# Performance work log

Measured on AMD Instinct MI355X. Metric: run time of the kernel, lower is better.

Reference implementation:

```python
import jax, jax.numpy as jnp
import numpy as np

HIDDEN = 512
BATCH = 32
SEQ = 4096


def setup_inputs() -> dict:
    key = jax.random.key(0)
    ks = jax.random.split(key, 8)
    s = 1.0 / np.sqrt(HIDDEN)
    return {
        "encoder_outputs": jax.random.normal(ks[0], (BATCH, SEQ, HIDDEN), jnp.float32),
        "decoder_hidden": jax.random.normal(ks[1], (BATCH, HIDDEN), jnp.float32),
        "W_enc": jax.random.uniform(ks[2], (HIDDEN, HIDDEN), jnp.float32, -s, s),
        "b_enc": jax.random.uniform(ks[3], (HIDDEN,), jnp.float32, -s, s),
        "W_dec": jax.random.uniform(ks[4], (HIDDEN, HIDDEN), jnp.float32, -s, s),
        "b_dec": jax.random.uniform(ks[5], (HIDDEN,), jnp.float32, -s, s),
        "W_v": jax.random.uniform(ks[6], (HIDDEN, 1), jnp.float32, -s, s),
        "b_v": jax.random.uniform(ks[7], (1,), jnp.float32, -s, s),
    }


def reference(encoder_outputs, decoder_hidden, W_enc, b_enc, W_dec, b_dec, W_v, b_v):
    # (b, s, h) projected encoder states
    enc_proj = jnp.einsum("bsh,hk->bsk", encoder_outputs, W_enc) + b_enc
    # (b, 1, h) projected decoder state, broadcast-added over seq
    dec_proj = (decoder_hidden @ W_dec + b_dec)[:, None, :]
    # score: (b, s, 1)
    score = jnp.tanh(enc_proj + dec_proj) @ W_v + b_v
    attention_weights = jax.nn.softmax(score, axis=1)  # softmax over seq_len
    # context: (b, h) weighted sum of encoder outputs
    context = jnp.sum(attention_weights * encoder_outputs, axis=1)
    return context, jnp.squeeze(attention_weights, -1)
```

## Files before the change

kernel.cpp:

```cpp
#include <hip/hip_runtime.h>
#include <hip/hip_bf16.h>

typedef __attribute__((ext_vector_type(8))) short bf16x8;
typedef __attribute__((ext_vector_type(4))) float f32x4;

#define HID 512
#define NB 32
#define SEQL 4096
#define BM 64
#define BK 32
#define NKC 16
#define NBLK 2048

#define WS_BP    0
#define WS_DPROJ (512*1024)
#define WS_SUM   (576*1024)

__device__ __forceinline__ short f2bf(float f) {
    unsigned u = __float_as_uint(f);
    unsigned r = (u + 0x7fffu + ((u >> 16) & 1u)) >> 16;
    return (short)r;
}

__device__ __forceinline__ float fast_tanh(float x) {
    float e = __expf(2.0f * x);
    float r = __builtin_amdgcn_rcpf(e + 1.0f);
    return 1.0f - 2.0f * r;
}

__device__ __forceinline__ void async16(const void* g, void* l) {
    __builtin_amdgcn_global_load_lds((__attribute__((address_space(1))) void*)(g),
                                     (__attribute__((address_space(3))) void*)(l),
                                     16, 0, 0);
}

__global__ void k_pre(const float* __restrict__ We, short* __restrict__ Bp,
                      const float* __restrict__ dec, const float* __restrict__ Wd,
                      const float* __restrict__ be, const float* __restrict__ bd,
                      float* __restrict__ dproj, float* __restrict__ out,
                      float* __restrict__ sumacc) {
    const int blk = blockIdx.x, t = threadIdx.x;
    if (blk < 128) {
        int tid  = blk * 256 + t;
        int lane = tid & 63;
        int nt   = (tid >> 6) & 31;
        int kc   = tid >> 11;
        int k0   = kc * 32 + (lane >> 4) * 8;
        int n    = nt * 16 + (lane & 15);
        bf16x8 v;
#pragma unroll
        for (int j = 0; j < 8; ++j) v[j] = f2bf(We[(size_t)(k0 + j) * HID + n]);
        *(bf16x8*)&Bp[(size_t)tid * 8] = v;
    } else if (blk < 192) {
        int bid = blk - 128;
        if (bid == 0 && t < NB) sumacc[t] = 0.f;
        int kl = t & 31, bq = t >> 5;
        int k  = (bid & 15) * 32 + kl;
        int b  = (bid >> 4) * 8 + bq;
        float a = be[k] + bd[k];
        const float* dr = dec + (size_t)b * HID;
#pragma unroll 8
        for (int h = 0; h < HID; ++h)
            a += dr[h] * Wd[(size_t)h * HID + k];
        dproj[(size_t)b * HID + k] = a;
    } else {
        out[(blk - 192) * 256 + t] = 0.f;
    }
}

__global__ __launch_bounds__(256, 2)
void k_main(const float* __restrict__ E, const short* __restrict__ Bp,
            const float* __restrict__ dproj, const float* __restrict__ Wv,
            float* __restrict__ out, float* __restrict__ sumacc) {
    __shared__ short As[2][BM][BK + 8];
    __shared__ short Bs[2][BK * HID];
    __shared__ float fbuf[640];
    __shared__ float pbuf[BM];

    const int tid  = threadIdx.x;
    const int wave = tid >> 6, lane = tid & 63;
    const int quad = lane >> 4, l15 = lane & 15;
    const int bid  = blockIdx.x;
    const int row0 = bid * BM;
    const int b    = bid >> 6;

    f32x4 acc[4][8];
#pragma unroll
    for (int r = 0; r < 4; ++r)
#pragma unroll
        for (int c = 0; c < 8; ++c) acc[r][c] = (f32x4){0.f, 0.f, 0.f, 0.f};

    const int arow = tid >> 2, akq = tid & 3;
    const float* aptr = E + (size_t)(row0 + arow) * HID + akq * 8;

    {
        const short* bsrc = Bp;
#pragma unroll
        for (int i = 0; i < 8; ++i) {
            int off = (i * 4 + wave) * 512;
            async16(bsrc + off + lane * 8, &Bs[0][off]);
        }
        float4 a0 = *(const float4*)(aptr);
        float4 a1 = *(const float4*)(aptr + 4);
        bf16x8 av;
        av[0] = f2bf(a0.x); av[1] = f2bf(a0.y); av[2] = f2bf(a0.z); av[3] = f2bf(a0.w);
        av[4] = f2bf(a1.x); av[5] = f2bf(a1.y); av[6] = f2bf(a1.z); av[7] = f2bf(a1.w);
        *(bf16x8*)&As[0][arow][akq * 8] = av;
    }

    int cur = 0;
    for (int kc = 0; kc < NKC; ++kc) {
        const int nxt = cur ^ 1;
        __syncthreads();

        float4 a0, a1;
        const bool pf = (kc + 1 < NKC);
        if (pf) {
            a0 = *(const float4*)(aptr + (kc + 1) * 32);
            a1 = *(const float4*)(aptr + (kc + 1) * 32 + 4);
            const short* bsrc = Bp + (size_t)(kc + 1) * 16384;
#pragma unroll
            for (int i = 0; i < 8; ++i) {
                int off = (i * 4 + wave) * 512;
                async16(bsrc + off + lane * 8, &Bs[nxt][off]);
            }
        }

        bf16x8 fa[4];
#pragma unroll
        for (int r = 0; r < 4; ++r) fa[r] = *(bf16x8*)&As[cur][r * 16 + l15][quad * 8];
#pragma unroll
        for (int c = 0; c < 8; ++c) {
            int nt = wave * 8 + c;
            bf16x8 fb = *(bf16x8*)&Bs[cur][(nt * 64 + lane) * 8];
#pragma unroll
            for (int r = 0; r < 4; ++r)
                acc[r][c] = __builtin_amdgcn_mfma_f32_16x16x32_bf16(fa[r], fb, acc[r][c], 0, 0, 0);
        }

        if (pf) {
            bf16x8 av;
            av[0] = f2bf(a0.x); av[1] = f2bf(a0.y); av[2] = f2bf(a0.z); av[3] = f2bf(a0.w);
            av[4] = f2bf(a1.x); av[5] = f2bf(a1.y); av[6] = f2bf(a1.z); av[7] = f2bf(a1.w);
            *(bf16x8*)&As[nxt][arow][akq * 8] = av;
        }
        cur = nxt;
    }

    float part[4][4];
#pragma unroll
    for (int r = 0; r < 4; ++r)
#pragma unroll
        for (int g = 0; g < 4; ++g) part[r][g] = 0.f;
    const float* dp = dproj + (size_t)b * HID;
#pragma unroll
    for (int c = 0; c < 8; ++c) {
        int col = wave * 128 + c * 16 + l15;
        float dv = dp[col];
        float wv = Wv[col];
#pragma unroll
        for (int r = 0; r < 4; ++r)
#pragma unroll
            for (int g = 0; g < 4; ++g)
                part[r][g] += fast_tanh(acc[r][c][g] + dv) * wv;
    }
#pragma unroll
    for (int r = 0; r < 4; ++r)
#pragma unroll
        for (int g = 0; g < 4; ++g) {
            float v = part[r][g];
            v += __shfl_xor(v, 1); v += __shfl_xor(v, 2);
            v += __shfl_xor(v, 4); v += __shfl_xor(v, 8);
            part[r][g] = v;
        }
    if (l15 == 0) {
#pragma unroll
        for (int r = 0; r < 4; ++r)
#pragma unroll
            for (int g = 0; g < 4; ++g)
                fbuf[wave * 64 + r * 16 + quad * 4 + g] = part[r][g];
    }
    __syncthreads();
    if (tid < 64) {
        float s  = fbuf[tid] + fbuf[64 + tid] + fbuf[128 + tid] + fbuf[192 + tid];
        float pv = __expf(s);
        pbuf[tid] = pv;
        out[(size_t)NB * HID + row0 + tid] = pv;
        float t2 = pv;
        t2 += __shfl_xor(t2, 1);  t2 += __shfl_xor(t2, 2);  t2 += __shfl_xor(t2, 4);
        t2 += __shfl_xor(t2, 8);  t2 += __shfl_xor(t2, 16); t2 += __shfl_xor(t2, 32);
        if (tid == 0) atomicAdd(&sumacc[b], t2);
    }
    __syncthreads();

    const int hq = tid & 127, rh = tid >> 7;
    const float4* E4 = (const float4*)E;
    size_t cbase = (size_t)(row0 + rh * 32) * (HID / 4) + hq;
    float4 ca = {0.f, 0.f, 0.f, 0.f};
#pragma unroll 4
    for (int rr = 0; rr < 32; ++rr) {
        float w  = pbuf[rh * 32 + rr];
        float4 e = E4[cbase + (size_t)rr * (HID / 4)];
        ca.x += w * e.x; ca.y += w * e.y; ca.z += w * e.z; ca.w += w * e.w;
    }
    if (rh == 1) {
        fbuf[hq] = ca.x; fbuf[128 + hq] = ca.y; fbuf[256 + hq] = ca.z; fbuf[384 + hq] = ca.w;
    }
    __syncthreads();
    if (rh == 0) {
        ca.x += fbuf[hq]; ca.y += fbuf[128 + hq]; ca.z += fbuf[256 + hq]; ca.w += fbuf[384 + hq];
        float* cg = out + (size_t)b * HID + hq * 4;
        atomicAdd(cg + 0, ca.x); atomicAdd(cg + 1, ca.y);
        atomicAdd(cg + 2, ca.z); atomicAdd(cg + 3, ca.w);
    }
}

__global__ void k_finish(float* __restrict__ out, const float* __restrict__ sumacc) {
    int b = blockIdx.x, t = threadIdx.x;
    float rs = 1.0f / sumacc[b];
    for (int i = t; i < HID; i += 256)
        out[(size_t)b * HID + i] *= rs;
    float* ow = out + (size_t)NB * HID + (size_t)b * SEQL;
    for (int i = t; i < SEQL; i += 256)
        ow[i] *= rs;
}

extern "C" void kernel_launch(void* const* d_in, const int* in_sizes, int n_in,
                              void* d_out, int out_size, void* d_ws, size_t ws_size,
                              hipStream_t stream) {
    const float* E   = (const float*)d_in[0];
    const float* dec = (const float*)d_in[1];
    const float* We  = (const float*)d_in[2];
    const float* be  = (const float*)d_in[3];
    const float* Wd  = (const float*)d_in[4];
    const float* bd  = (const float*)d_in[5];
    const float* Wv  = (const float*)d_in[6];
    float* out = (float*)d_out;
    char*  ws  = (char*)d_ws;
    short* Bp     = (short*)(ws + WS_BP);
    float* dproj  = (float*)(ws + WS_DPROJ);
    float* sumacc = (float*)(ws + WS_SUM);

    k_pre<<<256, 256, 0, stream>>>(We, Bp, dec, Wd, be, bd, dproj, out, sumacc);
    k_main<<<NBLK, 256, 0, stream>>>(E, Bp, dproj, Wv, out, sumacc);
    k_finish<<<NB, 256, 0, stream>>>(out, sumacc);
}
```

Baseline: 492.0 us.

## Deepen encoder-tile prefetch to two stages and split decoder projection across more blocks

The main GEMM loop now keeps two register stages of encoder loads in flight, issuing the load for chunk kc+2 while chunk kc is computed, and fully unrolls the k-loop so the buffer indices are compile-time constants. The decoder projection in the prep kernel is split over 512 blocks, with each block reducing its hidden dimension across 8 thread groups through shared memory, replacing 64 blocks that each ran a serial 512-long dot product. The aim is to hide global-load latency in the main kernel and shorten the prep kernel's critical path. The cost is more live registers, which could hurt occupancy at 2 blocks per CU, plus one redundant wrap-around load of chunk 0 in the last iterations.

```diff
diff --git a/kernel.cpp b/kernel.cpp
--- a/kernel.cpp
+++ b/kernel.cpp
@@ -51,20 +51,31 @@
 #pragma unroll
         for (int j = 0; j < 8; ++j) v[j] = f2bf(We[(size_t)(k0 + j) * HID + n]);
         *(bf16x8*)&Bp[(size_t)tid * 8] = v;
-    } else if (blk < 192) {
-        int bid = blk - 128;
-        if (bid == 0 && t < NB) sumacc[t] = 0.f;
-        int kl = t & 31, bq = t >> 5;
-        int k  = (bid & 15) * 32 + kl;
-        int b  = (bid >> 4) * 8 + bq;
-        float a = be[k] + bd[k];
+    } else if (blk < 640) {
+        __shared__ float red[8][33];
+        int bid2 = blk - 128;
+        int b  = bid2 >> 4, kg = bid2 & 15;
+        int kl = t & 31,    hc = t >> 5;
+        int k  = kg * 32 + kl;
         const float* dr = dec + (size_t)b * HID;
+        float a = 0.f;
 #pragma unroll 8
-        for (int h = 0; h < HID; ++h)
+        for (int j = 0; j < 64; ++j) {
+            int h = hc * 64 + j;
             a += dr[h] * Wd[(size_t)h * HID + k];
-        dproj[(size_t)b * HID + k] = a;
+        }
+        red[hc][kl] = a;
+        __syncthreads();
+        if (hc == 0) {
+            float s = be[k] + bd[k];
+#pragma unroll
+            for (int c = 0; c < 8; ++c) s += red[c][kl];
+            dproj[(size_t)b * HID + k] = s;
+        }
     } else {
-        out[(blk - 192) * 256 + t] = 0.f;
+        int bz = blk - 640;
+        out[bz * 256 + t] = 0.f;
+        if (bz == 0 && t < NB) sumacc[t] = 0.f;
     }
 }
 
@@ -93,6 +104,12 @@
     const int arow = tid >> 2, akq = tid & 3;
     const float* aptr = E + (size_t)(row0 + arow) * HID + akq * 8;
 
+    float4 pa0[2], pa1[2];
+
+    pa0[0] = *(const float4*)(aptr);
+    pa1[0] = *(const float4*)(aptr + 4);
+    pa0[1] = *(const float4*)(aptr + 32);
+    pa1[1] = *(const float4*)(aptr + 36);
     {
         const short* bsrc = Bp;
 #pragma unroll
@@ -100,24 +117,23 @@
             int off = (i * 4 + wave) * 512;
             async16(bsrc + off + lane * 8, &Bs[0][off]);
         }
-        float4 a0 = *(const float4*)(aptr);
-        float4 a1 = *(const float4*)(aptr + 4);
         bf16x8 av;
-        av[0] = f2bf(a0.x); av[1] = f2bf(a0.y); av[2] = f2bf(a0.z); av[3] = f2bf(a0.w);
-        av[4] = f2bf(a1.x); av[5] = f2bf(a1.y); av[6] = f2bf(a1.z); av[7] = f2bf(a1.w);
+        av[0] = f2bf(pa0[0].x); av[1] = f2bf(pa0[0].y); av[2] = f2bf(pa0[0].z); av[3] = f2bf(pa0[0].w);
+        av[4] = f2bf(pa1[0].x); av[5] = f2bf(pa1[0].y); av[6] = f2bf(pa1[0].z); av[7] = f2bf(pa1[0].w);
         *(bf16x8*)&As[0][arow][akq * 8] = av;
     }
 
-    int cur = 0;
+#pragma unroll
     for (int kc = 0; kc < NKC; ++kc) {
-        const int nxt = cur ^ 1;
+        const int cur = kc & 1, nxt = cur ^ 1;
         __syncthreads();
 
-        float4 a0, a1;
-        const bool pf = (kc + 1 < NKC);
-        if (pf) {
-            a0 = *(const float4*)(aptr + (kc + 1) * 32);
-            a1 = *(const float4*)(aptr + (kc + 1) * 32 + 4);
+        {
+            const int src = (kc + 2 < NKC) ? (kc + 2) : 0;
+            pa0[kc & 1] = *(const float4*)(aptr + src * 32);
+            pa1[kc & 1] = *(const float4*)(aptr + src * 32 + 4);
+        }
+        if (kc + 1 < NKC) {
             const short* bsrc = Bp + (size_t)(kc + 1) * 16384;
 #pragma unroll
             for (int i = 0; i < 8; ++i) {
@@ -138,13 +154,13 @@
                 acc[r][c] = __builtin_amdgcn_mfma_f32_16x16x32_bf16(fa[r], fb, acc[r][c], 0, 0, 0);
         }
 
-        if (pf) {
+        if (kc + 1 < NKC) {
+            float4 a0 = pa0[nxt], a1 = pa1[nxt];
             bf16x8 av;
             av[0] = f2bf(a0.x); av[1] = f2bf(a0.y); av[2] = f2bf(a0.z); av[3] = f2bf(a0.w);
             av[4] = f2bf(a1.x); av[5] = f2bf(a1.y); av[6] = f2bf(a1.z); av[7] = f2bf(a1.w);
             *(bf16x8*)&As[nxt][arow][akq * 8] = av;
         }
-        cur = nxt;
     }
 
     float part[4][4];
@@ -241,7 +257,7 @@
     float* dproj  = (float*)(ws + WS_DPROJ);
     float* sumacc = (float*)(ws + WS_SUM);
 
-    k_pre<<<256, 256, 0, stream>>>(We, Bp, dec, Wd, be, bd, dproj, out, sumacc);
+    k_pre<<<704, 256, 0, stream>>>(We, Bp, dec, Wd, be, bd, dproj, out, sumacc);
     k_main<<<NBLK, 256, 0, stream>>>(E, Bp, dproj, Wv, out, sumacc);
     k_finish<<<NB, 256, 0, stream>>>(out, sumacc);
 }
```

Measured after the change: 478.3 us. -2.8%, faster.
